# Kernel tuning notes

Hardware: AMD Instinct MI355X
Metric: run time of the kernel (lower is better)

The kernel has to match this reference:

```python
import jax, jax.numpy as jnp
import numpy as np

N_NODES = 50000
N_EDGES = 800000
D_IN = 64
D_OUT = 64


def setup_inputs() -> dict:
    key = jax.random.key(0)
    k1, k2, k3 = jax.random.split(key, 3)
    features = jax.random.normal(k1, (N_NODES, D_IN), dtype=jnp.float32)
    W = jax.random.normal(k2, (D_IN, D_OUT), dtype=jnp.float32) * (1.0 / np.sqrt(D_IN))
    b = jnp.zeros((D_OUT,), dtype=jnp.float32)
    edge_index = jax.random.randint(k3, (2, N_EDGES), 0, N_NODES, dtype=jnp.int64)
    return {"features": features, "W": W, "b": b, "edge_index": edge_index}


def reference(features, W, b, edge_index):
    # PyG GCNConv: add self-loops, symmetric normalization D^{-1/2}(A+I)D^{-1/2},
    # then aggregate x[row] at col (source -> target), plus linear + bias.
    N = features.shape[0]
    loop = jnp.arange(N, dtype=edge_index.dtype)
    row = jnp.concatenate([edge_index[0], loop])  # source nodes
    col = jnp.concatenate([edge_index[1], loop])  # target nodes

    ones = jnp.ones(row.shape[0], dtype=features.dtype)
    deg = jax.ops.segment_sum(ones, col, num_segments=N)  # in-degree incl. self-loop
    dinv = jnp.where(deg > 0, jax.lax.rsqrt(deg), 0.0)
    norm = dinv[row] * dinv[col]  # [E+N]

    x = features @ W                          # [N, D_OUT], tiny GEMM
    msg = x[row] * norm[:, None]              # gather + scale  [E+N, D_OUT]
    out = jax.ops.segment_sum(msg, col, num_segments=N)  # scatter-add
    return out + b
```

## Files before the change

### kernel.cpp

```cpp
#include <hip/hip_runtime.h>
#include <hip/hip_fp16.h>

#define NN 50000
#define NE 800000
#define D  64
#define NBUK  256
#define NBLKS 500
#define CHUNK2 1600
#define HSTR  512
#define FS 68
#define GEMMB 782
#define CAP 8192

typedef float __attribute__((ext_vector_type(4))) f32x4;

__device__ inline int block_exscan(int val, int tid) {
    __shared__ int wsum[4];
    int lane = tid & 63, w = tid >> 6;
    int v = val;
    #pragma unroll
    for (int d = 1; d < 64; d <<= 1) {
        int t = __shfl_up(v, d);
        if (lane >= d) v += t;
    }
    if (lane == 63) wsum[w] = v;
    __syncthreads();
    int base = 0;
    #pragma unroll
    for (int i = 0; i < 4; ++i) base += (i < w) ? wsum[i] : 0;
    __syncthreads();
    return base + v - val;
}

__global__ __launch_bounds__(256) void k_hist_gemm(const int* __restrict__ col,
                                                   int* __restrict__ H,
                                                   const float* __restrict__ feat,
                                                   const float* __restrict__ W,
                                                   __half* __restrict__ y) {
    __shared__ float smem[64 * FS + D * D];
    const int tid = threadIdx.x;

    if (blockIdx.x < NBLKS) {
        int* h = reinterpret_cast<int*>(smem);
        const int blk = blockIdx.x;
        h[tid] = 0;
        __syncthreads();
        const uint4* col4 = reinterpret_cast<const uint4*>(col + blk * CHUNK2);
        for (int i = tid; i < CHUNK2 / 4; i += 256) {
            uint4 v = col4[i];
            atomicAdd(&h[v.x >> 8], 1);
            atomicAdd(&h[v.y >> 8], 1);
            atomicAdd(&h[v.z >> 8], 1);
            atomicAdd(&h[v.w >> 8], 1);
        }
        __syncthreads();
        H[tid * HSTR + blk] = h[tid];
        return;
    }

    float* feat_lds = smem;
    float* W_lds    = smem + 64 * FS;
    const int rbase = (blockIdx.x - NBLKS) * 64;

    {
        const float4* W4  = reinterpret_cast<const float4*>(W);
        float4*       Wl4 = reinterpret_cast<float4*>(W_lds);
        for (int i = tid; i < D * D / 4; i += 256) Wl4[i] = W4[i];
    }
    {
        const int k0 = (tid & 15) * 4;
        #pragma unroll
        for (int it = 0; it < 4; ++it) {
            int r  = it * 16 + (tid >> 4);
            int gr = rbase + r;
            float4 v = make_float4(0.f, 0.f, 0.f, 0.f);
            if (gr < NN) v = *reinterpret_cast<const float4*>(&feat[gr * D + k0]);
            *reinterpret_cast<float4*>(&feat_lds[r * FS + k0]) = v;
        }
    }
    __syncthreads();

    const int tx = tid & 15;
    const int ty = tid >> 4;

    float acc[4][4] = {};

    #pragma unroll 8
    for (int k = 0; k < D; ++k) {
        float4 w = *reinterpret_cast<const float4*>(&W_lds[k * D + tx * 4]);
        float f0 = feat_lds[(ty * 4 + 0) * FS + k];
        float f1 = feat_lds[(ty * 4 + 1) * FS + k];
        float f2 = feat_lds[(ty * 4 + 2) * FS + k];
        float f3 = feat_lds[(ty * 4 + 3) * FS + k];
        acc[0][0] = fmaf(f0, w.x, acc[0][0]); acc[0][1] = fmaf(f0, w.y, acc[0][1]);
        acc[0][2] = fmaf(f0, w.z, acc[0][2]); acc[0][3] = fmaf(f0, w.w, acc[0][3]);
        acc[1][0] = fmaf(f1, w.x, acc[1][0]); acc[1][1] = fmaf(f1, w.y, acc[1][1]);
        acc[1][2] = fmaf(f1, w.z, acc[1][2]); acc[1][3] = fmaf(f1, w.w, acc[1][3]);
        acc[2][0] = fmaf(f2, w.x, acc[2][0]); acc[2][1] = fmaf(f2, w.y, acc[2][1]);
        acc[2][2] = fmaf(f2, w.z, acc[2][2]); acc[2][3] = fmaf(f2, w.w, acc[2][3]);
        acc[3][0] = fmaf(f3, w.x, acc[3][0]); acc[3][1] = fmaf(f3, w.y, acc[3][1]);
        acc[3][2] = fmaf(f3, w.z, acc[3][2]); acc[3][3] = fmaf(f3, w.w, acc[3][3]);
    }

    #pragma unroll
    for (int i = 0; i < 4; ++i) {
        int gr = rbase + ty * 4 + i;
        if (gr < NN) {
            __half2 h0 = __floats2half2_rn(acc[i][0], acc[i][1]);
            __half2 h1 = __floats2half2_rn(acc[i][2], acc[i][3]);
            union { __half2 h[2]; uint2 u; } p;
            p.h[0] = h0; p.h[1] = h1;
            *reinterpret_cast<uint2*>(&y[gr * D + tx * 4]) = p.u;
        }
    }
}

__global__ __launch_bounds__(256) void k_scanA(int* __restrict__ H,
                                               int* __restrict__ bsum) {
    const int tid = threadIdx.x, bkt = blockIdx.x;
    int* Hb = H + bkt * HSTR;
    int v0 = 0, v1 = 0;
    if (tid < 250) { v0 = Hb[2 * tid]; v1 = Hb[2 * tid + 1]; }
    int sum = v0 + v1;
    int ex = block_exscan(sum, tid);
    if (tid < 250) { Hb[2 * tid] = ex; Hb[2 * tid + 1] = ex + v0; }
    if (tid == 255) bsum[bkt] = ex;
}

__global__ __launch_bounds__(256) void k_bucket(const int* __restrict__ row,
                                                const int* __restrict__ col,
                                                const int* __restrict__ H,
                                                const int* __restrict__ bsum,
                                                unsigned int* __restrict__ packed) {
    __shared__ int base_l[NBUK];
    __shared__ int rank[NBUK];
    const int tid = threadIdx.x, blk = blockIdx.x;
    int ex = block_exscan(bsum[tid], tid);
    base_l[tid] = ex + H[tid * HSTR + blk];
    rank[tid] = 0;
    __syncthreads();
    const uint4* col4 = reinterpret_cast<const uint4*>(col + blk * CHUNK2);
    const uint4* row4 = reinterpret_cast<const uint4*>(row + blk * CHUNK2);
    for (int i = tid; i < CHUNK2 / 4; i += 256) {
        uint4 c4 = col4[i];
        uint4 r4 = row4[i];
        #pragma unroll
        for (int e = 0; e < 4; ++e) {
            unsigned c = (e == 0) ? c4.x : (e == 1) ? c4.y : (e == 2) ? c4.z : c4.w;
            unsigned r = (e == 0) ? r4.x : (e == 1) ? r4.y : (e == 2) ? r4.z : r4.w;
            int bk = c >> 8;
            int rk = atomicAdd(&rank[bk], 1);
            packed[base_l[bk] + rk] = (r & 0xFFFF) | ((c & 0xFF) << 16);
        }
    }
}

__global__ __launch_bounds__(256) void k_csr(const unsigned int* __restrict__ packed,
                                             const int* __restrict__ bsum,
                                             int* __restrict__ off,
                                             int* __restrict__ cnt,
                                             float* __restrict__ dinv,
                                             unsigned short* __restrict__ csr) {
    __shared__ unsigned pk[CAP];
    __shared__ unsigned short lcsr[CAP];
    __shared__ int ncnt[NBUK];
    __shared__ int nbase[NBUK];
    __shared__ int rk2[NBUK];
    __shared__ int sstart;
    const int tid = threadIdx.x, b = blockIdx.x;

    int ex = block_exscan(bsum[tid], tid);
    if (tid == b) sstart = ex;
    ncnt[tid] = 0;
    rk2[tid] = 0;
    __syncthreads();

    const int start = sstart;
    const int size  = bsum[b];

    if (size <= CAP) {
        for (int i = tid; i < size; i += 256) pk[i] = packed[start + i];
        __syncthreads();
        for (int i = tid; i < size; i += 256)
            atomicAdd(&ncnt[(pk[i] >> 16) & 0xFF], 1);
        __syncthreads();
        int v2  = ncnt[tid];
        int ex2 = block_exscan(v2, tid);
        const int node = b * NBUK + tid;
        off[node]  = start + ex2;
        cnt[node]  = v2;
        dinv[node] = rsqrtf((float)v2 + 1.0f);
        nbase[tid] = ex2;
        __syncthreads();
        for (int i = tid; i < size; i += 256) {
            unsigned u = pk[i];
            int ln = (u >> 16) & 0xFF;
            int rk = atomicAdd(&rk2[ln], 1);
            lcsr[nbase[ln] + rk] = (unsigned short)(u & 0xFFFF);
        }
        __syncthreads();
        for (int i = tid; i < size; i += 256) csr[start + i] = lcsr[i];
    } else {
        for (int i = tid; i < size; i += 256)
            atomicAdd(&ncnt[(packed[start + i] >> 16) & 0xFF], 1);
        __syncthreads();
        int v2  = ncnt[tid];
        int ex2 = block_exscan(v2, tid);
        const int node = b * NBUK + tid;
        off[node]  = start + ex2;
        cnt[node]  = v2;
        dinv[node] = rsqrtf((float)v2 + 1.0f);
        nbase[tid] = start + ex2;
        __syncthreads();
        for (int i = tid; i < size; i += 256) {
            unsigned u = packed[start + i];
            int ln = (u >> 16) & 0xFF;
            int rk = atomicAdd(&rk2[ln], 1);
            csr[nbase[ln] + rk] = (unsigned short)(u & 0xFFFF);
        }
    }
}

__global__ __launch_bounds__(256, 8) void k_agg8(const unsigned short* __restrict__ csr,
                                                 const int* __restrict__ off,
                                                 const int* __restrict__ cnt,
                                                 const float* __restrict__ dinv,
                                                 const __half* __restrict__ y,
                                                 const float* __restrict__ b,
                                                 float* __restrict__ out) {
    const int lane = threadIdx.x & 63;
    const int g    = lane >> 3;
    const int l8   = lane & 7;
    const int wave = blockIdx.x * 4 + (threadIdx.x >> 6);
    const int c    = wave * 8 + g;
    const bool valid = (c < NN);

    const uint4* y16 = reinterpret_cast<const uint4*>(y);

    const int s = valid ? off[c] : 0;
    const int n = valid ? cnt[c] : 0;
    const float dc = valid ? dinv[c] : 0.0f;

    int pre0 = (l8      < n) ? (int)csr[s + l8     ] : 0;
    int pre1 = (l8 + 8  < n) ? (int)csr[s + l8 + 8 ] : 0;
    int pre2 = (l8 + 16 < n) ? (int)csr[s + l8 + 16] : 0;
    int pre3 = (l8 + 24 < n) ? (int)csr[s + l8 + 24] : 0;

    float acc[8] = {0.f, 0.f, 0.f, 0.f, 0.f, 0.f, 0.f, 0.f};

    auto addm = [&](uint4 u, float m) {
        const __half2* h = reinterpret_cast<const __half2*>(&u);
        float2 f0 = __half22float2(h[0]);
        float2 f1 = __half22float2(h[1]);
        float2 f2 = __half22float2(h[2]);
        float2 f3 = __half22float2(h[3]);
        acc[0] = fmaf(m, f0.x, acc[0]); acc[1] = fmaf(m, f0.y, acc[1]);
        acc[2] = fmaf(m, f1.x, acc[2]); acc[3] = fmaf(m, f1.y, acc[3]);
        acc[4] = fmaf(m, f2.x, acc[4]); acc[5] = fmaf(m, f2.y, acc[5]);
        acc[6] = fmaf(m, f3.x, acc[6]); acc[7] = fmaf(m, f3.y, acc[7]);
    };

    if (valid) addm(y16[c * 8 + l8], dc);

    const int srcb = lane & 56;

    #pragma unroll
    for (int w = 0; w < 4; ++w) {
        if (w * 8 < n) {
            const int pw = (w == 0) ? pre0 : (w == 1) ? pre1
                         : (w == 2) ? pre2 : pre3;
            uint4 u[8];
            float msk[8];
            #pragma unroll
            for (int e = 0; e < 8; ++e) {
                int r = __shfl(pw, srcb + e);
                u[e] = y16[r * 8 + l8];
                float dv = dinv[r];
                msk[e] = (w * 8 + e < n) ? dv : 0.0f;
            }
            #pragma unroll
            for (int e = 0; e < 8; ++e) addm(u[e], msk[e]);
        }
    }

    for (int i = 32; i < n; ++i) {
        int r = (int)csr[s + i];
        addm(y16[r * 8 + l8], dinv[r]);
    }

    if (valid) {
        const float4* b4 = reinterpret_cast<const float4*>(b);
        float4 bb0 = b4[l8 * 2], bb1 = b4[l8 * 2 + 1];
        f32x4 o0, o1;
        o0.x = acc[0] * dc + bb0.x;  o0.y = acc[1] * dc + bb0.y;
        o0.z = acc[2] * dc + bb0.z;  o0.w = acc[3] * dc + bb0.w;
        o1.x = acc[4] * dc + bb1.x;  o1.y = acc[5] * dc + bb1.y;
        o1.z = acc[6] * dc + bb1.z;  o1.w = acc[7] * dc + bb1.w;
        f32x4* out4 = reinterpret_cast<f32x4*>(out);
        __builtin_nontemporal_store(o0, &out4[c * 16 + l8 * 2]);
        __builtin_nontemporal_store(o1, &out4[c * 16 + l8 * 2 + 1]);
    }
}

extern "C" void kernel_launch(void* const* d_in, const int* in_sizes, int n_in,
                              void* d_out, int out_size, void* d_ws, size_t ws_size,
                              hipStream_t stream) {
    const float* feat = (const float*)d_in[0];
    const float* W    = (const float*)d_in[1];
    const float* b    = (const float*)d_in[2];
    const int*   ei   = (const int*)d_in[3];
    const int*   row  = ei;
    const int*   col  = ei + NE;

    float* out = (float*)d_out;

    int*            H      = (int*)d_ws;
    int*            bsum   = H + NBUK * HSTR;
    int*            cnt    = bsum + 1024;
    int*            off    = cnt + 65536;
    float*          dinv   = (float*)(off + 65536);
    unsigned int*   packed = (unsigned int*)(dinv + 65536);
    unsigned short* csr    = (unsigned short*)(packed + NE);
    __half*         y      = (__half*)(csr + NE);

    k_hist_gemm<<<NBLKS + GEMMB, 256, 0, stream>>>(col, H, feat, W, y);
    k_scanA    <<<NBUK,  256, 0, stream>>>(H, bsum);
    k_bucket   <<<NBLKS, 256, 0, stream>>>(row, col, H, bsum, packed);
    k_csr      <<<NBUK,  256, 0, stream>>>(packed, bsum, off, cnt, dinv, csr);
    k_agg8     <<<(NN + 31) / 32, 256, 0, stream>>>(csr, off, cnt, dinv, y, b, out);
}
```

Before: 53.87 us.

## Replace histogram scan with fixed-capacity buckets using global atomic cursors

Merges the bucketing pass into the histogram/GEMM kernel by reserving per-bucket slots with a global atomicAdd on a cursor array, with each bucket given a fixed capacity. This removes the scan kernel and the separate bucket kernel, cutting launches and a global pass over the edge arrays. It adds a memset and assumes no bucket exceeds the fixed capacity, silently dropping edges if one does. Edge order within a bucket becomes nondeterministic.

```diff
diff --git a/kernel.cpp b/kernel.cpp
--- a/kernel.cpp
+++ b/kernel.cpp
@@ -7,10 +7,9 @@
 #define NBUK  256
 #define NBLKS 500
 #define CHUNK2 1600
-#define HSTR  512
 #define FS 68
 #define GEMMB 782
-#define CAP 8192
+#define BCAP 4608
 
 typedef float __attribute__((ext_vector_type(4))) f32x4;
 
@@ -32,20 +31,25 @@
     return base + v - val;
 }
 
-__global__ __launch_bounds__(256) void k_hist_gemm(const int* __restrict__ col,
-                                                   int* __restrict__ H,
-                                                   const float* __restrict__ feat,
-                                                   const float* __restrict__ W,
-                                                   __half* __restrict__ y) {
+__global__ __launch_bounds__(256) void k_gemm_bucket(const int* __restrict__ row,
+                                                     const int* __restrict__ col,
+                                                     int* __restrict__ gcur,
+                                                     unsigned int* __restrict__ packed,
+                                                     const float* __restrict__ feat,
+                                                     const float* __restrict__ W,
+                                                     __half* __restrict__ y) {
     __shared__ float smem[64 * FS + D * D];
     const int tid = threadIdx.x;
 
     if (blockIdx.x < NBLKS) {
-        int* h = reinterpret_cast<int*>(smem);
+        int* h      = reinterpret_cast<int*>(smem);
+        int* base_l = h + NBUK;
+        int* rank   = base_l + NBUK;
         const int blk = blockIdx.x;
         h[tid] = 0;
         __syncthreads();
         const uint4* col4 = reinterpret_cast<const uint4*>(col + blk * CHUNK2);
+        const uint4* row4 = reinterpret_cast<const uint4*>(row + blk * CHUNK2);
         for (int i = tid; i < CHUNK2 / 4; i += 256) {
             uint4 v = col4[i];
             atomicAdd(&h[v.x >> 8], 1);
@@ -54,7 +58,21 @@
             atomicAdd(&h[v.w >> 8], 1);
         }
         __syncthreads();
-        H[tid * HSTR + blk] = h[tid];
+        base_l[tid] = tid * BCAP + atomicAdd(&gcur[tid], h[tid]);
+        rank[tid] = 0;
+        __syncthreads();
+        for (int i = tid; i < CHUNK2 / 4; i += 256) {
+            uint4 c4 = col4[i];
+            uint4 r4 = row4[i];
+            #pragma unroll
+            for (int e = 0; e < 4; ++e) {
+                unsigned c = (e == 0) ? c4.x : (e == 1) ? c4.y : (e == 2) ? c4.z : c4.w;
+                unsigned r = (e == 0) ? r4.x : (e == 1) ? r4.y : (e == 2) ? r4.z : r4.w;
+                int bk = c >> 8;
+                int rk = atomicAdd(&rank[bk], 1);
+                packed[base_l[bk] + rk] = (r & 0xFFFF) | ((c & 0xFF) << 16);
+            }
+        }
         return;
     }
 
@@ -115,110 +133,46 @@
     }
 }
 
-__global__ __launch_bounds__(256) void k_scanA(int* __restrict__ H,
-                                               int* __restrict__ bsum) {
-    const int tid = threadIdx.x, bkt = blockIdx.x;
-    int* Hb = H + bkt * HSTR;
-    int v0 = 0, v1 = 0;
-    if (tid < 250) { v0 = Hb[2 * tid]; v1 = Hb[2 * tid + 1]; }
-    int sum = v0 + v1;
-    int ex = block_exscan(sum, tid);
-    if (tid < 250) { Hb[2 * tid] = ex; Hb[2 * tid + 1] = ex + v0; }
-    if (tid == 255) bsum[bkt] = ex;
-}
-
-__global__ __launch_bounds__(256) void k_bucket(const int* __restrict__ row,
-                                                const int* __restrict__ col,
-                                                const int* __restrict__ H,
-                                                const int* __restrict__ bsum,
-                                                unsigned int* __restrict__ packed) {
-    __shared__ int base_l[NBUK];
-    __shared__ int rank[NBUK];
-    const int tid = threadIdx.x, blk = blockIdx.x;
-    int ex = block_exscan(bsum[tid], tid);
-    base_l[tid] = ex + H[tid * HSTR + blk];
-    rank[tid] = 0;
-    __syncthreads();
-    const uint4* col4 = reinterpret_cast<const uint4*>(col + blk * CHUNK2);
-    const uint4* row4 = reinterpret_cast<const uint4*>(row + blk * CHUNK2);
-    for (int i = tid; i < CHUNK2 / 4; i += 256) {
-        uint4 c4 = col4[i];
-        uint4 r4 = row4[i];
-        #pragma unroll
-        for (int e = 0; e < 4; ++e) {
-            unsigned c = (e == 0) ? c4.x : (e == 1) ? c4.y : (e == 2) ? c4.z : c4.w;
-            unsigned r = (e == 0) ? r4.x : (e == 1) ? r4.y : (e == 2) ? r4.z : r4.w;
-            int bk = c >> 8;
-            int rk = atomicAdd(&rank[bk], 1);
-            packed[base_l[bk] + rk] = (r & 0xFFFF) | ((c & 0xFF) << 16);
-        }
-    }
-}
-
 __global__ __launch_bounds__(256) void k_csr(const unsigned int* __restrict__ packed,
-                                             const int* __restrict__ bsum,
+                                             const int* __restrict__ gcur,
                                              int* __restrict__ off,
                                              int* __restrict__ cnt,
                                              float* __restrict__ dinv,
                                              unsigned short* __restrict__ csr) {
-    __shared__ unsigned pk[CAP];
-    __shared__ unsigned short lcsr[CAP];
+    __shared__ unsigned pk[BCAP];
+    __shared__ unsigned short lcsr[BCAP];
     __shared__ int ncnt[NBUK];
     __shared__ int nbase[NBUK];
     __shared__ int rk2[NBUK];
-    __shared__ int sstart;
     const int tid = threadIdx.x, b = blockIdx.x;
-
-    int ex = block_exscan(bsum[tid], tid);
-    if (tid == b) sstart = ex;
+    const int start = b * BCAP;
+    const int size  = min(gcur[b], BCAP);
+
     ncnt[tid] = 0;
     rk2[tid] = 0;
     __syncthreads();
 
-    const int start = sstart;
-    const int size  = bsum[b];
-
-    if (size <= CAP) {
-        for (int i = tid; i < size; i += 256) pk[i] = packed[start + i];
-        __syncthreads();
-        for (int i = tid; i < size; i += 256)
-            atomicAdd(&ncnt[(pk[i] >> 16) & 0xFF], 1);
-        __syncthreads();
-        int v2  = ncnt[tid];
-        int ex2 = block_exscan(v2, tid);
-        const int node = b * NBUK + tid;
-        off[node]  = start + ex2;
-        cnt[node]  = v2;
-        dinv[node] = rsqrtf((float)v2 + 1.0f);
-        nbase[tid] = ex2;
-        __syncthreads();
-        for (int i = tid; i < size; i += 256) {
-            unsigned u = pk[i];
-            int ln = (u >> 16) & 0xFF;
-            int rk = atomicAdd(&rk2[ln], 1);
-            lcsr[nbase[ln] + rk] = (unsigned short)(u & 0xFFFF);
-        }
-        __syncthreads();
-        for (int i = tid; i < size; i += 256) csr[start + i] = lcsr[i];
-    } else {
-        for (int i = tid; i < size; i += 256)
-            atomicAdd(&ncnt[(packed[start + i] >> 16) & 0xFF], 1);
-        __syncthreads();
-        int v2  = ncnt[tid];
-        int ex2 = block_exscan(v2, tid);
-        const int node = b * NBUK + tid;
-        off[node]  = start + ex2;
-        cnt[node]  = v2;
-        dinv[node] = rsqrtf((float)v2 + 1.0f);
-        nbase[tid] = start + ex2;
-        __syncthreads();
-        for (int i = tid; i < size; i += 256) {
-            unsigned u = packed[start + i];
-            int ln = (u >> 16) & 0xFF;
-            int rk = atomicAdd(&rk2[ln], 1);
-            csr[nbase[ln] + rk] = (unsigned short)(u & 0xFFFF);
-        }
-    }
+    for (int i = tid; i < size; i += 256) pk[i] = packed[start + i];
+    __syncthreads();
+    for (int i = tid; i < size; i += 256)
+        atomicAdd(&ncnt[(pk[i] >> 16) & 0xFF], 1);
+    __syncthreads();
+    int v2  = ncnt[tid];
+    int ex2 = block_exscan(v2, tid);
+    const int node = b * NBUK + tid;
+    off[node]  = start + ex2;
+    cnt[node]  = v2;
+    dinv[node] = rsqrtf((float)v2 + 1.0f);
+    nbase[tid] = ex2;
+    __syncthreads();
+    for (int i = tid; i < size; i += 256) {
+        unsigned u = pk[i];
+        int ln = (u >> 16) & 0xFF;
+        int rk = atomicAdd(&rk2[ln], 1);
+        lcsr[nbase[ln] + rk] = (unsigned short)(u & 0xFFFF);
+    }
+    __syncthreads();
+    for (int i = tid; i < size; i += 256) csr[start + i] = lcsr[i];
 }
 
 __global__ __launch_bounds__(256, 8) void k_agg8(const unsigned short* __restrict__ csr,
@@ -314,18 +268,18 @@
 
     float* out = (float*)d_out;
 
-    int*            H      = (int*)d_ws;
-    int*            bsum   = H + NBUK * HSTR;
-    int*            cnt    = bsum + 1024;
+    int*            gcur   = (int*)d_ws;
+    int*            cnt    = gcur + 1024;
     int*            off    = cnt + 65536;
     float*          dinv   = (float*)(off + 65536);
     unsigned int*   packed = (unsigned int*)(dinv + 65536);
-    unsigned short* csr    = (unsigned short*)(packed + NE);
-    __half*         y      = (__half*)(csr + NE);
-
-    k_hist_gemm<<<NBLKS + GEMMB, 256, 0, stream>>>(col, H, feat, W, y);
-    k_scanA    <<<NBUK,  256, 0, stream>>>(H, bsum);
-    k_bucket   <<<NBLKS, 256, 0, stream>>>(row, col, H, bsum, packed);
-    k_csr      <<<NBUK,  256, 0, stream>>>(packed, bsum, off, cnt, dinv, csr);
-    k_agg8     <<<(NN + 31) / 32, 256, 0, stream>>>(csr, off, cnt, dinv, y, b, out);
-}
+    unsigned short* csr    = (unsigned short*)(packed + NBUK * BCAP);
+    __half*         y      = (__half*)(csr + NBUK * BCAP);
+
+    hipMemsetAsync(gcur, 0, NBUK * sizeof(int), stream);
+
+    k_gemm_bucket<<<NBLKS + GEMMB, 256, 0, stream>>>(row, col, gcur, packed,
+                                                     feat, W, y);
+    k_csr <<<NBUK, 256, 0, stream>>>(packed, gcur, off, cnt, dinv, csr);
+    k_agg8<<<(NN + 31) / 32, 256, 0, stream>>>(csr, off, cnt, dinv, y, b, out);
+}
```

Result: slower. 57.07 us (+6.0%).

## Halve edge chunk size and remap chunks across XCDs for histogram and bucketing

Applied to the files above, without the earlier changes.

Doubles the number of histogram/bucketing blocks by halving the edge chunk each block processes, so more workgroups are in flight on the GPU. It also adds a block-to-chunk permutation that interleaves chunks by blockIdx&7, so consecutive chunks land on the same XCD and scatter writes from neighbouring chunks stay in one XCD's L2. The scan kernel now processes four histogram entries per thread. Costs are twice as many per-block LDS histogram init and flush passes and a larger H array. With 200 iterations per block the 256-thread blocks are underfilled.

```diff
diff --git a/kernel.cpp b/kernel.cpp
--- a/kernel.cpp
+++ b/kernel.cpp
@@ -5,14 +5,16 @@
 #define NE 800000
 #define D  64
 #define NBUK  256
-#define NBLKS 500
-#define CHUNK2 1600
-#define HSTR  512
+#define NBLKS 1000
+#define CHUNK2 800
+#define HSTR  1024
 #define FS 68
 #define GEMMB 782
 #define CAP 8192
 
 typedef float __attribute__((ext_vector_type(4))) f32x4;
+
+__device__ __forceinline__ int chunk_of(int b) { return (b & 7) * 125 + (b >> 3); }
 
 __device__ inline int block_exscan(int val, int tid) {
     __shared__ int wsum[4];
@@ -42,10 +44,10 @@
 
     if (blockIdx.x < NBLKS) {
         int* h = reinterpret_cast<int*>(smem);
-        const int blk = blockIdx.x;
+        const int chunk = chunk_of(blockIdx.x);
         h[tid] = 0;
         __syncthreads();
-        const uint4* col4 = reinterpret_cast<const uint4*>(col + blk * CHUNK2);
+        const uint4* col4 = reinterpret_cast<const uint4*>(col + chunk * CHUNK2);
         for (int i = tid; i < CHUNK2 / 4; i += 256) {
             uint4 v = col4[i];
             atomicAdd(&h[v.x >> 8], 1);
@@ -54,7 +56,7 @@
             atomicAdd(&h[v.w >> 8], 1);
         }
         __syncthreads();
-        H[tid * HSTR + blk] = h[tid];
+        H[tid * HSTR + chunk] = h[tid];
         return;
     }
 
@@ -119,11 +121,19 @@
                                                int* __restrict__ bsum) {
     const int tid = threadIdx.x, bkt = blockIdx.x;
     int* Hb = H + bkt * HSTR;
-    int v0 = 0, v1 = 0;
-    if (tid < 250) { v0 = Hb[2 * tid]; v1 = Hb[2 * tid + 1]; }
-    int sum = v0 + v1;
+    int v0 = 0, v1 = 0, v2 = 0, v3 = 0;
+    if (tid < 250) {
+        v0 = Hb[4 * tid];     v1 = Hb[4 * tid + 1];
+        v2 = Hb[4 * tid + 2]; v3 = Hb[4 * tid + 3];
+    }
+    int sum = v0 + v1 + v2 + v3;
     int ex = block_exscan(sum, tid);
-    if (tid < 250) { Hb[2 * tid] = ex; Hb[2 * tid + 1] = ex + v0; }
+    if (tid < 250) {
+        Hb[4 * tid]     = ex;
+        Hb[4 * tid + 1] = ex + v0;
+        Hb[4 * tid + 2] = ex + v0 + v1;
+        Hb[4 * tid + 3] = ex + v0 + v1 + v2;
+    }
     if (tid == 255) bsum[bkt] = ex;
 }
 
@@ -134,13 +144,14 @@
                                                 unsigned int* __restrict__ packed) {
     __shared__ int base_l[NBUK];
     __shared__ int rank[NBUK];
-    const int tid = threadIdx.x, blk = blockIdx.x;
+    const int tid = threadIdx.x;
+    const int chunk = chunk_of(blockIdx.x);
     int ex = block_exscan(bsum[tid], tid);
-    base_l[tid] = ex + H[tid * HSTR + blk];
+    base_l[tid] = ex + H[tid * HSTR + chunk];
     rank[tid] = 0;
     __syncthreads();
-    const uint4* col4 = reinterpret_cast<const uint4*>(col + blk * CHUNK2);
-    const uint4* row4 = reinterpret_cast<const uint4*>(row + blk * CHUNK2);
+    const uint4* col4 = reinterpret_cast<const uint4*>(col + chunk * CHUNK2);
+    const uint4* row4 = reinterpret_cast<const uint4*>(row + chunk * CHUNK2);
     for (int i = tid; i < CHUNK2 / 4; i += 256) {
         uint4 c4 = col4[i];
         uint4 r4 = row4[i];
```

New measurement: 53.94 us. Within noise of the previous version (+0.1%).
